# Optimization experiments

Hardware: AMD Instinct MI355X
Metric: run time of the kernel (lower is better)

## Reference

```python
import jax, jax.numpy as jnp
from jax import lax
import numpy as np

B, T, N_IN, N_HID, N_OUT = 256, 500, 128, 512, 64


def setup_inputs() -> dict:
    key = jax.random.key(0)
    ks = jax.random.split(key, 7)
    # modest scales so relu recurrence stays stable over 500 steps
    return {
        "input_signal": jax.random.normal(ks[0], (B, T, N_IN), jnp.float32),
        "hidden": jnp.zeros((B, N_HID), jnp.float32),
        "W_ih": jax.random.normal(ks[1], (N_HID, N_IN), jnp.float32) * (1.0 / np.sqrt(N_IN)),
        "W_hh": jax.random.normal(ks[2], (N_HID, N_HID), jnp.float32) * (0.5 / np.sqrt(N_HID)),
        "b_ih": jax.random.normal(ks[3], (N_HID,), jnp.float32) * 0.01,
        "b_hh": jax.random.normal(ks[4], (N_HID,), jnp.float32) * 0.01,
        "W_out": jax.random.normal(ks[5], (N_OUT, N_HID), jnp.float32) * (1.0 / np.sqrt(N_HID)),
        "b_out": jnp.zeros((N_OUT,), jnp.float32),
        # alpha = self.alpha(torch.Tensor([1])) == alpha Linear weight column: per-unit leak
        "alpha": jnp.asarray(np.array([0.1] * 50 + [0.4] * (N_HID - 50)), jnp.float32),
    }


def reference(input_signal, hidden, W_ih, W_hh, b_ih, b_hh, W_out, b_out, alpha):
    # input_signal: [B, T, n_in] -> time-major [T, B, n_in]
    x_tm = jnp.swapaxes(input_signal, 0, 1)

    def step(h, x_t):
        # nn.RNNCell(relu): relu(x W_ih^T + b_ih + h W_hh^T + b_hh)
        cand = jax.nn.relu(x_t @ W_ih.T + b_ih + h @ W_hh.T + b_hh)
        h_new = (1.0 - alpha) * h + alpha * cand  # leaky integration, per-unit alpha
        return h_new, h_new

    h_final, hidden_seq = lax.scan(step, hidden, x_tm)  # hidden_seq: [T, B, n_hid]
    output_seq = hidden_seq @ W_out.T + b_out  # [T, B, n_out]
    hidden_list = jnp.swapaxes(hidden_seq, 0, 1)  # [B, T, n_hid]
    output_list = jnp.swapaxes(output_seq, 0, 1)  # [B, T, n_out]
    return hidden_list, output_list, h_final
```

## Files before the change

kernel.cpp:

```cpp
#include <hip/hip_runtime.h>
#include <stdint.h>
#include <stddef.h>

#define Bb   256
#define Tt   500
#define NIN  128
#define NH   512
#define NOUT 64

typedef __attribute__((ext_vector_type(8))) short  short8;
typedef __attribute__((ext_vector_type(4))) float  float4v;
typedef __attribute__((ext_vector_type(2))) float  float2v;

__device__ __forceinline__ unsigned short f2b(float f) {
    union { float f; unsigned u; } v; v.f = f;
    unsigned u = v.u;
    unsigned r = (u + 0x7FFFu + ((u >> 16) & 1u)) >> 16;
    return (unsigned short)r;
}

__device__ __forceinline__ short8 cvt8(const float* __restrict__ p) {
    const float4v a = *(const float4v*)p;
    const float4v b = *(const float4v*)(p + 4);
    short8 r;
    r[0] = (short)f2b(a[0]); r[1] = (short)f2b(a[1]);
    r[2] = (short)f2b(a[2]); r[3] = (short)f2b(a[3]);
    r[4] = (short)f2b(b[0]); r[5] = (short)f2b(b[1]);
    r[6] = (short)f2b(b[2]); r[7] = (short)f2b(b[3]);
    return r;
}

__device__ __forceinline__ short8 ld_frag_cp(const unsigned short* p) {
    unsigned long long lo = __hip_atomic_load((const unsigned long long*)p,
                                              __ATOMIC_RELAXED, __HIP_MEMORY_SCOPE_AGENT);
    unsigned long long hi = __hip_atomic_load((const unsigned long long*)(p + 4),
                                              __ATOMIC_RELAXED, __HIP_MEMORY_SCOPE_AGENT);
    union { unsigned long long u[2]; short8 s; } v;
    v.u[0] = lo; v.u[1] = hi;
    return v.s;
}

__global__ void init_flags_kernel(unsigned int* flags) {
    flags[threadIdx.x] = 0u;
}

__global__ void __launch_bounds__(256) rnn_persist(
    const float* __restrict__ x,
    const float* __restrict__ h0,
    const float* __restrict__ Wih,
    const float* __restrict__ Whh,
    const float* __restrict__ bih,
    const float* __restrict__ bhh,
    const float* __restrict__ alpha,
    float* __restrict__ out,
    unsigned short* __restrict__ Hx,
    unsigned int* __restrict__ flags)
{
    const int wg  = blockIdx.x;
    const int g   = wg & 15;
    const int s   = wg >> 4;
    const int r0  = g << 4;
    const int c0  = s << 5;
    const int tid = threadIdx.x;
    const int w   = tid >> 6;
    const int l   = tid & 63;
    const int l15 = l & 15;
    const int q   = l >> 4;

    __shared__ float Cred[4 * 2 * 4 * 16 * 4];

    short8 fw_hh[2][4], fw_ih[2];
    for (int nt = 0; nt < 2; ++nt) {
        for (int i = 0; i < 4; ++i) {
            const float* p = Whh + (size_t)(c0 + nt * 16 + l15) * NH
                                 + (4 * w + i) * 32 + q * 8;
            fw_hh[nt][i] = cvt8(p);
        }
        fw_ih[nt] = cvt8(Wih + (size_t)(c0 + nt * 16 + l15) * NIN + w * 32 + q * 8);
    }

    const int urow = tid >> 4;
    const int ucol = (tid & 15) * 2;
    const int gb   = r0 + urow;
    float hcur0 = h0[(size_t)gb * NH + c0 + ucol];
    float hcur1 = h0[(size_t)gb * NH + c0 + ucol + 1];
    const float bias0 = bih[c0 + ucol]     + bhh[c0 + ucol];
    const float bias1 = bih[c0 + ucol + 1] + bhh[c0 + ucol + 1];
    const float al0 = alpha[c0 + ucol], al1 = alpha[c0 + ucol + 1];

    float* hid_out   = out;
    float* final_out = out + (size_t)Bb * Tt * NH + (size_t)Bb * Tt * NOUT;

    unsigned int* gflags = flags + g * 16;

    for (int t = 0; t < Tt; ++t) {
        const short8 ax = cvt8(x + ((size_t)(r0 + l15) * Tt + t) * NIN + w * 32 + q * 8);

        if (t > 0) {
            if (tid < 16) {
                const unsigned int* fp = gflags + tid;
                while (__hip_atomic_load(fp, __ATOMIC_RELAXED,
                                         __HIP_MEMORY_SCOPE_AGENT) < (unsigned)t)
                    __builtin_amdgcn_s_sleep(1);
            }
            __syncthreads();
        }

        short8 ah[4];
        if (t == 0) {
            for (int i = 0; i < 4; ++i)
                ah[i] = cvt8(h0 + (size_t)(r0 + l15) * NH + (4 * w + i) * 32 + q * 8);
        } else {
            const unsigned short* hb = Hx + (size_t)((t - 1) & 1) * Bb * NH
                                          + (size_t)(r0 + l15) * NH;
            for (int i = 0; i < 4; ++i)
                ah[i] = ld_frag_cp(hb + (4 * w + i) * 32 + q * 8);
        }

        for (int nt = 0; nt < 2; ++nt) {
            float4v acc = {0.f, 0.f, 0.f, 0.f};
            for (int i = 0; i < 4; ++i)
                acc = __builtin_amdgcn_mfma_f32_16x16x32_bf16(ah[i], fw_hh[nt][i], acc, 0, 0, 0);
            acc = __builtin_amdgcn_mfma_f32_16x16x32_bf16(ax, fw_ih[nt], acc, 0, 0, 0);
            *(float4v*)&Cred[(((w * 2 + nt) * 4 + q) * 16 + l15) * 4] = acc;
        }
        __syncthreads();

        const int nt0 = ucol >> 4,       n0 = ucol & 15;
        const int nt1 = (ucol + 1) >> 4, n1 = (ucol + 1) & 15;
        const int qq = urow >> 2, rr = urow & 3;
        float s0 = 0.f, s1 = 0.f;
        for (int ww = 0; ww < 4; ++ww) {
            s0 += Cred[(((ww * 2 + nt0) * 4 + qq) * 16 + n0) * 4 + rr];
            s1 += Cred[(((ww * 2 + nt1) * 4 + qq) * 16 + n1) * 4 + rr];
        }
        float cand0 = s0 + bias0; cand0 = cand0 > 0.f ? cand0 : 0.f;
        float cand1 = s1 + bias1; cand1 = cand1 > 0.f ? cand1 : 0.f;
        hcur0 = (1.f - al0) * hcur0 + al0 * cand0;
        hcur1 = (1.f - al1) * hcur1 + al1 * cand1;

        const unsigned int packed = (unsigned)f2b(hcur0) | ((unsigned)f2b(hcur1) << 16);
        __hip_atomic_store(
            (unsigned int*)(Hx + (size_t)(t & 1) * Bb * NH + (size_t)gb * NH + c0 + ucol),
            packed, __ATOMIC_RELAXED, __HIP_MEMORY_SCOPE_AGENT);

        asm volatile("s_waitcnt vmcnt(0)" ::: "memory");
        __syncthreads();
        if (tid == 0)
            __hip_atomic_store(gflags + s, (unsigned)(t + 1),
                               __ATOMIC_RELAXED, __HIP_MEMORY_SCOPE_AGENT);

        const float2v hv = {hcur0, hcur1};
        *(float2v*)(hid_out + ((size_t)gb * Tt + t) * NH + c0 + ucol) = hv;
        if (t == Tt - 1)
            *(float2v*)(final_out + (size_t)gb * NH + c0 + ucol) = hv;
    }
}

__global__ void __launch_bounds__(256) out_proj(
    const float* __restrict__ hid,
    const float* __restrict__ Wout,
    const float* __restrict__ bout,
    float* __restrict__ outp)
{
    const int tid = threadIdx.x;
    const int w = tid >> 6, l = tid & 63, l15 = l & 15, q = l >> 4;
    const size_t rid0 = (size_t)blockIdx.x * 64;

    short8 fb[16];
    for (int kc = 0; kc < 16; ++kc)
        fb[kc] = cvt8(Wout + (size_t)(w * 16 + l15) * NH + kc * 32 + q * 8);
    const float bv = bout[w * 16 + l15];

    for (int rs = 0; rs < 4; ++rs) {
        float4v acc = {bv, bv, bv, bv};
        const float* ap = hid + (rid0 + rs * 16 + l15) * NH + q * 8;
        for (int kc = 0; kc < 16; ++kc)
            acc = __builtin_amdgcn_mfma_f32_16x16x32_bf16(cvt8(ap + kc * 32), fb[kc], acc, 0, 0, 0);
        for (int r = 0; r < 4; ++r) {
            size_t rid = rid0 + rs * 16 + q * 4 + r;
            outp[rid * NOUT + w * 16 + l15] = acc[r];
        }
    }
}

extern "C" void kernel_launch(void* const* d_in, const int* in_sizes, int n_in,
                              void* d_out, int out_size, void* d_ws, size_t ws_size,
                              hipStream_t stream) {
    (void)in_sizes; (void)n_in; (void)out_size; (void)ws_size;
    const float* x     = (const float*)d_in[0];
    const float* h0    = (const float*)d_in[1];
    const float* Wih   = (const float*)d_in[2];
    const float* Whh   = (const float*)d_in[3];
    const float* bih   = (const float*)d_in[4];
    const float* bhh   = (const float*)d_in[5];
    const float* Wout  = (const float*)d_in[6];
    const float* bout  = (const float*)d_in[7];
    const float* alpha = (const float*)d_in[8];
    float* out = (float*)d_out;

    unsigned short* Hx   = (unsigned short*)d_ws;
    unsigned int*  flags = (unsigned int*)((char*)d_ws + (size_t)2 * Bb * NH * 2);

    init_flags_kernel<<<1, 256, 0, stream>>>(flags);

    void* args[] = { (void*)&x, (void*)&h0, (void*)&Wih, (void*)&Whh,
                     (void*)&bih, (void*)&bhh, (void*)&alpha, (void*)&out,
                     (void*)&Hx, (void*)&flags };
    hipLaunchCooperativeKernel((const void*)rnn_persist, dim3(256), dim3(256),
                               args, 0, stream);

    const float* hid = out;
    float* outp = out + (size_t)Bb * Tt * NH;
    out_proj<<<2000, 256, 0, stream>>>(hid, Wout, bout, outp);
}
```

Measured before the change: 1.870 ms.

## Fuse output projection into persistent RNN kernel and use per-wave sync flags

```diff
diff --git a/kernel.cpp b/kernel.cpp
--- a/kernel.cpp
+++ b/kernel.cpp
@@ -41,7 +41,7 @@
 }
 
 __global__ void init_flags_kernel(unsigned int* flags) {
-    flags[threadIdx.x] = 0u;
+    flags[blockIdx.x * 256 + threadIdx.x] = 0u;
 }
 
 __global__ void __launch_bounds__(256) rnn_persist(
@@ -52,6 +52,8 @@
     const float* __restrict__ bih,
     const float* __restrict__ bhh,
     const float* __restrict__ alpha,
+    const float* __restrict__ Wout,
+    const float* __restrict__ bout,
     float* __restrict__ out,
     unsigned short* __restrict__ Hx,
     unsigned int* __restrict__ flags)
@@ -66,10 +68,12 @@
     const int l   = tid & 63;
     const int l15 = l & 15;
     const int q   = l >> 4;
+    const bool do_out = (s < 4);
 
     __shared__ float Cred[4 * 2 * 4 * 16 * 4];
-
-    short8 fw_hh[2][4], fw_ih[2];
+    __shared__ float Cred2[4 * 4 * 16 * 4];
+
+    short8 fw_hh[2][4], fw_ih[2], fw_out[4];
     for (int nt = 0; nt < 2; ++nt) {
         for (int i = 0; i < 4; ++i) {
             const float* p = Whh + (size_t)(c0 + nt * 16 + l15) * NH
@@ -78,33 +82,39 @@
         }
         fw_ih[nt] = cvt8(Wih + (size_t)(c0 + nt * 16 + l15) * NIN + w * 32 + q * 8);
     }
+    if (do_out) {
+        for (int i = 0; i < 4; ++i)
+            fw_out[i] = cvt8(Wout + (size_t)(s * 16 + l15) * NH + (4 * w + i) * 32 + q * 8);
+    }
 
     const int urow = tid >> 4;
     const int ucol = (tid & 15) * 2;
+    const int oc   = tid & 15;
     const int gb   = r0 + urow;
     float hcur0 = h0[(size_t)gb * NH + c0 + ucol];
     float hcur1 = h0[(size_t)gb * NH + c0 + ucol + 1];
     const float bias0 = bih[c0 + ucol]     + bhh[c0 + ucol];
     const float bias1 = bih[c0 + ucol + 1] + bhh[c0 + ucol + 1];
     const float al0 = alpha[c0 + ucol], al1 = alpha[c0 + ucol + 1];
+    const float ob  = do_out ? bout[s * 16 + oc] : 0.f;
 
     float* hid_out   = out;
-    float* final_out = out + (size_t)Bb * Tt * NH + (size_t)Bb * Tt * NOUT;
-
-    unsigned int* gflags = flags + g * 16;
+    float* outp      = out + (size_t)Bb * Tt * NH;
+    float* final_out = outp + (size_t)Bb * Tt * NOUT;
+
+    unsigned int* gflags = flags + g * 64;
+    const int myflag = s * 4 + w;
 
     for (int t = 0; t < Tt; ++t) {
         const short8 ax = cvt8(x + ((size_t)(r0 + l15) * Tt + t) * NIN + w * 32 + q * 8);
 
         if (t > 0) {
-            if (tid < 16) {
-                const unsigned int* fp = gflags + tid;
-                while (__hip_atomic_load(fp, __ATOMIC_RELAXED,
-                                         __HIP_MEMORY_SCOPE_AGENT) < (unsigned)t)
-                    __builtin_amdgcn_s_sleep(1);
-            }
-            __syncthreads();
-        }
+            const unsigned int* fp = gflags + l;
+            while (__hip_atomic_load(fp, __ATOMIC_RELAXED,
+                                     __HIP_MEMORY_SCOPE_AGENT) < (unsigned)t)
+                __builtin_amdgcn_s_sleep(1);
+        }
+        asm volatile("" ::: "memory");
 
         short8 ah[4];
         if (t == 0) {
@@ -123,6 +133,12 @@
                 acc = __builtin_amdgcn_mfma_f32_16x16x32_bf16(ah[i], fw_hh[nt][i], acc, 0, 0, 0);
             acc = __builtin_amdgcn_mfma_f32_16x16x32_bf16(ax, fw_ih[nt], acc, 0, 0, 0);
             *(float4v*)&Cred[(((w * 2 + nt) * 4 + q) * 16 + l15) * 4] = acc;
+        }
+        if (do_out) {
+            float4v acc2 = {0.f, 0.f, 0.f, 0.f};
+            for (int i = 0; i < 4; ++i)
+                acc2 = __builtin_amdgcn_mfma_f32_16x16x32_bf16(ah[i], fw_out[i], acc2, 0, 0, 0);
+            *(float4v*)&Cred2[((w * 4 + q) * 16 + l15) * 4] = acc2;
         }
         __syncthreads();
 
@@ -144,43 +160,47 @@
             (unsigned int*)(Hx + (size_t)(t & 1) * Bb * NH + (size_t)gb * NH + c0 + ucol),
             packed, __ATOMIC_RELAXED, __HIP_MEMORY_SCOPE_AGENT);
 
+        float oval = 0.f;
+        if (do_out) {
+            float so = 0.f;
+            for (int ww = 0; ww < 4; ++ww)
+                so += Cred2[((ww * 4 + qq) * 16 + oc) * 4 + rr];
+            oval = so + ob;
+        }
+
         asm volatile("s_waitcnt vmcnt(0)" ::: "memory");
-        __syncthreads();
-        if (tid == 0)
-            __hip_atomic_store(gflags + s, (unsigned)(t + 1),
-                               __ATOMIC_RELAXED, __HIP_MEMORY_SCOPE_AGENT);
+        if (l == 0)
+            __hip_atomic_store(gflags + myflag, (unsigned)(t + 1),
+                               __ATOMIC_RELEASE - __ATOMIC_RELEASE + __ATOMIC_RELAXED,
+                               __HIP_MEMORY_SCOPE_AGENT);
 
         const float2v hv = {hcur0, hcur1};
         *(float2v*)(hid_out + ((size_t)gb * Tt + t) * NH + c0 + ucol) = hv;
+        if (do_out && t > 0)
+            outp[((size_t)gb * Tt + (t - 1)) * NOUT + s * 16 + oc] = oval;
         if (t == Tt - 1)
             *(float2v*)(final_out + (size_t)gb * NH + c0 + ucol) = hv;
     }
-}
-
-__global__ void __launch_bounds__(256) out_proj(
-    const float* __restrict__ hid,
-    const float* __restrict__ Wout,
-    const float* __restrict__ bout,
-    float* __restrict__ outp)
-{
-    const int tid = threadIdx.x;
-    const int w = tid >> 6, l = tid & 63, l15 = l & 15, q = l >> 4;
-    const size_t rid0 = (size_t)blockIdx.x * 64;
-
-    short8 fb[16];
-    for (int kc = 0; kc < 16; ++kc)
-        fb[kc] = cvt8(Wout + (size_t)(w * 16 + l15) * NH + kc * 32 + q * 8);
-    const float bv = bout[w * 16 + l15];
-
-    for (int rs = 0; rs < 4; ++rs) {
-        float4v acc = {bv, bv, bv, bv};
-        const float* ap = hid + (rid0 + rs * 16 + l15) * NH + q * 8;
-        for (int kc = 0; kc < 16; ++kc)
-            acc = __builtin_amdgcn_mfma_f32_16x16x32_bf16(cvt8(ap + kc * 32), fb[kc], acc, 0, 0, 0);
-        for (int r = 0; r < 4; ++r) {
-            size_t rid = rid0 + rs * 16 + q * 4 + r;
-            outp[rid * NOUT + w * 16 + l15] = acc[r];
-        }
+
+    if (do_out) {
+        const unsigned int* fp = gflags + l;
+        while (__hip_atomic_load(fp, __ATOMIC_RELAXED,
+                                 __HIP_MEMORY_SCOPE_AGENT) < (unsigned)Tt)
+            __builtin_amdgcn_s_sleep(1);
+        asm volatile("" ::: "memory");
+        const unsigned short* hb = Hx + (size_t)((Tt - 1) & 1) * Bb * NH
+                                      + (size_t)(r0 + l15) * NH;
+        float4v acc2 = {0.f, 0.f, 0.f, 0.f};
+        for (int i = 0; i < 4; ++i)
+            acc2 = __builtin_amdgcn_mfma_f32_16x16x32_bf16(
+                       ld_frag_cp(hb + (4 * w + i) * 32 + q * 8), fw_out[i], acc2, 0, 0, 0);
+        *(float4v*)&Cred2[((w * 4 + q) * 16 + l15) * 4] = acc2;
+        __syncthreads();
+        const int qq = urow >> 2, rr = urow & 3;
+        float so = 0.f;
+        for (int ww = 0; ww < 4; ++ww)
+            so += Cred2[((ww * 4 + qq) * 16 + oc) * 4 + rr];
+        outp[((size_t)gb * Tt + (Tt - 1)) * NOUT + s * 16 + oc] = so + ob;
     }
 }
 
@@ -202,15 +222,12 @@
     unsigned short* Hx   = (unsigned short*)d_ws;
     unsigned int*  flags = (unsigned int*)((char*)d_ws + (size_t)2 * Bb * NH * 2);
 
-    init_flags_kernel<<<1, 256, 0, stream>>>(flags);
+    init_flags_kernel<<<4, 256, 0, stream>>>(flags);
 
     void* args[] = { (void*)&x, (void*)&h0, (void*)&Wih, (void*)&Whh,
-                     (void*)&bih, (void*)&bhh, (void*)&alpha, (void*)&out,
+                     (void*)&bih, (void*)&bhh, (void*)&alpha,
+                     (void*)&Wout, (void*)&bout, (void*)&out,
                      (void*)&Hx, (void*)&flags };
     hipLaunchCooperativeKernel((const void*)rnn_persist, dim3(256), dim3(256),
                                args, 0, stream);
-
-    const float* hid = out;
-    float* outp = out + (size_t)Bb * Tt * NH;
-    out_proj<<<2000, 256, 0, stream>>>(hid, Wout, bout, outp);
-}
+}
```

New measurement: 3.324 ms. +77.8%, slower.
